# Kernel tuning notes

Hardware: AMD Instinct MI355X
Metric: run time of the kernel (lower is better)

Reference implementation:

```python
import jax, jax.numpy as jnp
import numpy as np

MARGIN = 1.0


def setup_inputs() -> dict:
    key = jax.random.key(0)
    k1, k2, k3 = jax.random.split(key, 3)
    n, d = 8192, 128
    feat1 = jax.random.normal(k1, (n, d), dtype=jnp.float32)
    feat2 = jax.random.normal(k2, (n, d), dtype=jnp.float32)
    # similarity labels in {+1, -1}, as expected by HingeEmbeddingLoss
    simi = (2 * jax.random.randint(k3, (n, n), 0, 2) - 1).astype(jnp.int32)
    return {"feat1": feat1, "feat2": feat2, "simi": simi}


def reference(feat1, feat2, simi):
    # logits[i,j] = -||feat1_i - feat2_j||^2, computed without the O(n*m*d) expand
    sq1 = jnp.sum(feat1 * feat1, axis=-1, keepdims=True)          # [n, 1]
    sq2 = jnp.sum(feat2 * feat2, axis=-1)                          # [m]
    cross = jnp.einsum('nd,md->nm', feat1, feat2)                  # [n, m]
    logits = -(sq1 + sq2[None, :] - 2.0 * cross)                   # [n, m]
    probs = jax.nn.softmax(logits, axis=1)                         # [n, m]
    # HingeEmbeddingLoss: x if y==1 else max(0, margin - x); mean reduction
    loss = jnp.where(simi == 1, probs, jnp.maximum(0.0, MARGIN - probs))
    return jnp.mean(loss)
```

## Files before the change

kernel.cpp:

```cpp
#include <hip/hip_runtime.h>
#include <hip/hip_bf16.h>
#include <stdint.h>

#define N 8192
#define D 128
#define NCHUNK 16
#define CHUNK (N / NCHUNK)
#define RT 128
#define CT 64
#define NTILES (CHUNK / CT)
#define NBLK (N / RT * NCHUNK)

typedef short bf16x8 __attribute__((ext_vector_type(8)));
typedef float f32x4 __attribute__((ext_vector_type(4)));
typedef int   i32x4 __attribute__((ext_vector_type(4)));
typedef unsigned int uint32;

#define OFF_ACC   0u
#define OFF_SQ2   1024u
#define OFF_BCNT  (OFF_SQ2 + N * 4u)
#define OFF_M     (OFF_BCNT + NBLK * 4u)
#define OFF_L     (OFF_M + NCHUNK * N * 4u)
#define OFF_S     (OFF_L + NCHUNK * N * 4u)
#define OFF_F1    (OFF_S + NCHUNK * N * 4u)
#define OFF_F2    (OFF_F1 + N * D * 2u)

__global__ __launch_bounds__(256)
void prep_kernel(const float* __restrict__ f1, const float* __restrict__ f2,
                 unsigned short* __restrict__ f1b, unsigned short* __restrict__ f2b,
                 float* __restrict__ sq2) {
    const int w    = blockIdx.x * 4 + (threadIdx.x >> 6);
    const int lane = threadIdx.x & 63;
    for (int row = w; row < N; row += 1024) {
        float a0 = f1[row * D + lane];
        float a1 = f1[row * D + 64 + lane];
        float b0 = f2[row * D + lane];
        float b1 = f2[row * D + 64 + lane];
        __hip_bfloat16 t;
        t = __float2bfloat16(a0); f1b[row * D + lane]      = *(unsigned short*)&t;
        t = __float2bfloat16(a1); f1b[row * D + 64 + lane] = *(unsigned short*)&t;
        t = __float2bfloat16(b0); f2b[row * D + lane]      = *(unsigned short*)&t;
        t = __float2bfloat16(b1); f2b[row * D + 64 + lane] = *(unsigned short*)&t;
        float ss = b0 * b0 + b1 * b1;
        #pragma unroll
        for (int off = 32; off > 0; off >>= 1) ss += __shfl_xor(ss, off);
        if (lane == 0) sq2[row] = ss;
    }
}

__global__ __launch_bounds__(256)
void main_kernel(const unsigned short* __restrict__ f1b,
                 const unsigned short* __restrict__ f2b,
                 const float* __restrict__ sq2,
                 const int* __restrict__ simi,
                 float* __restrict__ pm, float* __restrict__ pl, float* __restrict__ ps,
                 uint32* __restrict__ blockcnt) {
    __shared__ uint32 cred[4];

    const int tid  = threadIdx.x;
    const int wave = tid >> 6;
    const int lane = tid & 63;
    const int lo   = lane & 15;
    const int hi   = lane >> 4;

    const int rowtile = blockIdx.x;
    const int chunk   = blockIdx.y;
    const int rbase   = rowtile * RT + wave * 32;
    const int cbase0  = chunk * CHUNK;

    bf16x8 afrag[2][4];
    #pragma unroll
    for (int a = 0; a < 2; a++) {
        const unsigned short* ap = f1b + (size_t)(rbase + a * 16 + lo) * D + hi * 8;
        #pragma unroll
        for (int kk = 0; kk < 4; kk++)
            afrag[a][kk] = *reinterpret_cast<const bf16x8*>(ap + kk * 32);
    }

    const int* simi_p = simi + (size_t)(rbase + hi * 4) * N + cbase0 + 4 * lo;
    const unsigned short* bp = f2b + (size_t)(cbase0 + 4 * lo) * D + hi * 8;

    float m[2][4], l[2][4], s[2][4];
    #pragma unroll
    for (int a = 0; a < 2; a++)
        #pragma unroll
        for (int r = 0; r < 4; r++) { m[a][r] = -1e30f; l[a][r] = 0.f; s[a][r] = 0.f; }
    uint32 cnt = 0;

    for (int t = 0; t < NTILES; t++) {
        i32x4 mkv[2][4];
        #pragma unroll
        for (int a = 0; a < 2; a++)
            #pragma unroll
            for (int r = 0; r < 4; r++)
                mkv[a][r] = __builtin_nontemporal_load(
                    reinterpret_cast<const i32x4*>(simi_p + (size_t)(a * 16 + r) * N));

        f32x4 acc[2][4];
        #pragma unroll
        for (int cf = 0; cf < 4; cf++) {
            acc[0][cf] = (f32x4){0.f, 0.f, 0.f, 0.f};
            acc[1][cf] = (f32x4){0.f, 0.f, 0.f, 0.f};
            #pragma unroll
            for (int kk = 0; kk < 4; kk++) {
                bf16x8 b = *reinterpret_cast<const bf16x8*>(bp + (size_t)cf * D + kk * 32);
                acc[0][cf] = __builtin_amdgcn_mfma_f32_16x16x32_bf16(afrag[0][kk], b, acc[0][cf], 0, 0, 0);
                acc[1][cf] = __builtin_amdgcn_mfma_f32_16x16x32_bf16(afrag[1][kk], b, acc[1][cf], 0, 0, 0);
            }
        }

        uint32 mb[2][4];
        #pragma unroll
        for (int a = 0; a < 2; a++)
            #pragma unroll
            for (int r = 0; r < 4; r++) {
                i32x4 v = mkv[a][r];
                uint32 nib = (uint32)(v[0] == 1) | ((uint32)(v[1] == 1) << 1) |
                             ((uint32)(v[2] == 1) << 2) | ((uint32)(v[3] == 1) << 3);
                mb[a][r] = nib;
                cnt += 4u - __popc(nib);
            }

        f32x4 sqv = *reinterpret_cast<const f32x4*>(sq2 + cbase0 + t * CT + 4 * lo);
        #pragma unroll
        for (int a = 0; a < 2; a++)
            #pragma unroll
            for (int r = 0; r < 4; r++) {
                float lg[4];
                #pragma unroll
                for (int cf = 0; cf < 4; cf++)
                    lg[cf] = 2.0f * acc[a][cf][r] - sqv[cf];
                float tm = fmaxf(fmaxf(lg[0], lg[1]), fmaxf(lg[2], lg[3]));
                float mn = fmaxf(m[a][r], tm);
                float al = __expf(m[a][r] - mn);
                m[a][r] = mn;
                float p[4];
                #pragma unroll
                for (int cf = 0; cf < 4; cf++) p[cf] = __expf(lg[cf] - mn);
                l[a][r] = l[a][r] * al + ((p[0] + p[1]) + (p[2] + p[3]));
                float sm = 0.f;
                #pragma unroll
                for (int cf = 0; cf < 4; cf++)
                    sm += ((mb[a][r] >> cf) & 1u) ? p[cf] : 0.f;
                s[a][r] = s[a][r] * al + sm;
            }
        simi_p += CT;
        bp += (size_t)CT * D;
    }

    #pragma unroll
    for (int a = 0; a < 2; a++)
        #pragma unroll
        for (int r = 0; r < 4; r++) {
            float M = m[a][r];
            #pragma unroll
            for (int off = 1; off < 16; off <<= 1)
                M = fmaxf(M, __shfl_xor(M, off));
            float sc = __expf(m[a][r] - M);
            float L = l[a][r] * sc, S = s[a][r] * sc;
            #pragma unroll
            for (int off = 1; off < 16; off <<= 1) {
                L += __shfl_xor(L, off);
                S += __shfl_xor(S, off);
            }
            if (lo == 0) {
                int row = rbase + a * 16 + hi * 4 + r;
                int idx = chunk * N + row;
                pm[idx] = M; pl[idx] = L; ps[idx] = S;
            }
        }

    #pragma unroll
    for (int off = 1; off < 64; off <<= 1) cnt += __shfl_xor(cnt, off);
    if (lane == 0) cred[wave] = cnt;
    __syncthreads();
    if (tid == 0)
        blockcnt[blockIdx.y * 64 + blockIdx.x] = cred[0] + cred[1] + cred[2] + cred[3];
}

__global__ void merge_kernel(const float* __restrict__ pm, const float* __restrict__ pl,
                             const float* __restrict__ ps, const uint32* __restrict__ blockcnt,
                             float* __restrict__ s_acc, uint32* __restrict__ neg_acc) {
    const int row = blockIdx.x * 256 + threadIdx.x;
    float M = -1e30f;
    #pragma unroll
    for (int k = 0; k < NCHUNK; k++) M = fmaxf(M, pm[k * N + row]);
    float L = 0.f, S = 0.f;
    #pragma unroll
    for (int k = 0; k < NCHUNK; k++) {
        float e = __expf(pm[k * N + row] - M);
        L += pl[k * N + row] * e;
        S += ps[k * N + row] * e;
    }
    float r = S / L;
    uint32 pc = (threadIdx.x < 32) ? blockcnt[blockIdx.x * 32 + threadIdx.x] : 0u;
    #pragma unroll
    for (int off = 32; off > 0; off >>= 1) {
        r  += __shfl_xor(r, off);
        pc += __shfl_xor(pc, off);
    }
    __shared__ float red[4];
    __shared__ uint32 redp[4];
    int lane = threadIdx.x & 63, w = threadIdx.x >> 6;
    if (lane == 0) { red[w] = r; redp[w] = pc; }
    __syncthreads();
    if (threadIdx.x == 0) {
        atomicAdd(s_acc, red[0] + red[1] + red[2] + red[3]);
        atomicAdd(neg_acc, redp[0] + redp[1] + redp[2] + redp[3]);
    }
}

__global__ void final_kernel(const float* __restrict__ s_acc, const uint32* __restrict__ neg_acc,
                             float* __restrict__ out) {
    double S = (double)s_acc[0];
    double C = (double)neg_acc[0];
    double n = (double)N;
    out[0] = (float)((2.0 * S + C - n) / (n * n));
}

extern "C" void kernel_launch(void* const* d_in, const int* in_sizes, int n_in,
                              void* d_out, int out_size, void* d_ws, size_t ws_size,
                              hipStream_t stream) {
    const float* f1   = (const float*)d_in[0];
    const float* f2   = (const float*)d_in[1];
    const int*   simi = (const int*)d_in[2];
    float* out = (float*)d_out;
    char* ws = (char*)d_ws;

    float*  acc_s    = (float*)(ws + OFF_ACC);
    uint32* acc_n    = (uint32*)(ws + OFF_ACC + 4);
    float*  sq2      = (float*)(ws + OFF_SQ2);
    uint32* blockcnt = (uint32*)(ws + OFF_BCNT);
    float*  pm       = (float*)(ws + OFF_M);
    float*  pl       = (float*)(ws + OFF_L);
    float*  ps       = (float*)(ws + OFF_S);
    unsigned short* f1b = (unsigned short*)(ws + OFF_F1);
    unsigned short* f2b = (unsigned short*)(ws + OFF_F2);

    hipMemsetAsync(ws + OFF_ACC, 0, 64, stream);
    prep_kernel<<<256, 256, 0, stream>>>(f1, f2, f1b, f2b, sq2);
    main_kernel<<<dim3(N / RT, NCHUNK), 256, 0, stream>>>(f1b, f2b, sq2, simi,
                                                          pm, pl, ps, blockcnt);
    merge_kernel<<<N / 256, 256, 0, stream>>>(pm, pl, ps, blockcnt, acc_s, acc_n);
    final_kernel<<<1, 1, 0, stream>>>(acc_s, acc_n, out);
}
```

Measured before the change: 446.6 us.

## Stage feat2 column tiles in double-buffered swizzled LDS shared across waves

Each wave used to load its own B fragments for feat2 straight from global memory. Now the block cooperatively loads each 64-column tile once into LDS with an XOR swizzle, and all four waves read their fragments from there. The next tile is prefetched into registers while the current one is computed, then written into the second LDS buffer. This removes redundant global and L2 traffic for B, at the cost of 32KB of LDS, a __syncthreads per tile and extra registers that may lower occupancy.

```diff
diff --git a/kernel.cpp b/kernel.cpp
--- a/kernel.cpp
+++ b/kernel.cpp
@@ -55,6 +55,7 @@
                  const int* __restrict__ simi,
                  float* __restrict__ pm, float* __restrict__ pl, float* __restrict__ ps,
                  uint32* __restrict__ blockcnt) {
+    __shared__ unsigned short ldsB[2][CT * D];
     __shared__ uint32 cred[4];
 
     const int tid  = threadIdx.x;
@@ -77,8 +78,10 @@
             afrag[a][kk] = *reinterpret_cast<const bf16x8*>(ap + kk * 32);
     }
 
+    const int sq_ = (tid >> 4);
+    const int sg_ = tid & 15;
+
     const int* simi_p = simi + (size_t)(rbase + hi * 4) * N + cbase0 + 4 * lo;
-    const unsigned short* bp = f2b + (size_t)(cbase0 + 4 * lo) * D + hi * 8;
 
     float m[2][4], l[2][4], s[2][4];
     #pragma unroll
@@ -87,7 +90,18 @@
         for (int r = 0; r < 4; r++) { m[a][r] = -1e30f; l[a][r] = 0.f; s[a][r] = 0.f; }
     uint32 cnt = 0;
 
+    #pragma unroll
+    for (int it = 0; it < 4; it++) {
+        int q = it * 16 + sq_;
+        int c = 4 * (q & 15) + (q >> 4);
+        uint4 v = *reinterpret_cast<const uint4*>(f2b + (size_t)(cbase0 + c) * D + sg_ * 8);
+        *reinterpret_cast<uint4*>(&ldsB[0][q * D + ((sg_ ^ (q & 15)) * 8)]) = v;
+    }
+    __syncthreads();
+
     for (int t = 0; t < NTILES; t++) {
+        const int cur = t & 1;
+
         i32x4 mkv[2][4];
         #pragma unroll
         for (int a = 0; a < 2; a++)
@@ -96,18 +110,34 @@
                 mkv[a][r] = __builtin_nontemporal_load(
                     reinterpret_cast<const i32x4*>(simi_p + (size_t)(a * 16 + r) * N));
 
+        uint4 stg[4];
+        if (t < NTILES - 1) {
+            const int cb_n = cbase0 + (t + 1) * CT;
+            #pragma unroll
+            for (int it = 0; it < 4; it++) {
+                int q = it * 16 + sq_;
+                int c = 4 * (q & 15) + (q >> 4);
+                stg[it] = *reinterpret_cast<const uint4*>(
+                    f2b + (size_t)(cb_n + c) * D + sg_ * 8);
+            }
+        }
+
         f32x4 acc[2][4];
         #pragma unroll
         for (int cf = 0; cf < 4; cf++) {
             acc[0][cf] = (f32x4){0.f, 0.f, 0.f, 0.f};
             acc[1][cf] = (f32x4){0.f, 0.f, 0.f, 0.f};
+            const int brow = cf * 16 + lo;
             #pragma unroll
             for (int kk = 0; kk < 4; kk++) {
-                bf16x8 b = *reinterpret_cast<const bf16x8*>(bp + (size_t)cf * D + kk * 32);
+                int g = kk * 4 + hi;
+                bf16x8 b = *reinterpret_cast<const bf16x8*>(
+                    &ldsB[cur][brow * D + ((g ^ (brow & 15)) * 8)]);
                 acc[0][cf] = __builtin_amdgcn_mfma_f32_16x16x32_bf16(afrag[0][kk], b, acc[0][cf], 0, 0, 0);
                 acc[1][cf] = __builtin_amdgcn_mfma_f32_16x16x32_bf16(afrag[1][kk], b, acc[1][cf], 0, 0, 0);
             }
         }
+        __builtin_amdgcn_sched_barrier(0);
 
         uint32 mb[2][4];
         #pragma unroll
@@ -144,8 +174,18 @@
                     sm += ((mb[a][r] >> cf) & 1u) ? p[cf] : 0.f;
                 s[a][r] = s[a][r] * al + sm;
             }
+
+        if (t < NTILES - 1) {
+            #pragma unroll
+            for (int it = 0; it < 4; it++) {
+                int q = it * 16 + sq_;
+                *reinterpret_cast<uint4*>(
+                    &ldsB[cur ^ 1][q * D + ((sg_ ^ (q & 15)) * 8)]) = stg[it];
+            }
+        }
+
+        __syncthreads();
         simi_p += CT;
-        bp += (size_t)CT * D;
     }
 
     #pragma unroll
```

Measured after the change: 390.5 us. -12.6%, faster.
